# Performance work log

Measured on AMD Instinct MI355X. Metric: run time of the kernel, lower is better.

The kernel has to match this reference:

```python
import jax, jax.numpy as jnp
import numpy as np

DIM = 1024
DFF = 4096
LN_EPS = 1e-5


def _layernorm(x, g, b):
    mu = jnp.mean(x, axis=-1, keepdims=True)
    var = jnp.mean((x - mu) ** 2, axis=-1, keepdims=True)
    return (x - mu) * jax.lax.rsqrt(var + LN_EPS) * g + b


def setup_inputs() -> dict:
    key = jax.random.key(0)
    ks = jax.random.split(key, 16)
    B, L, D, F = 4, 2048, DIM, DFF
    return {
        "x": jax.random.normal(ks[0], (B, L, D), dtype=jnp.float32),
        "hidden_real": jax.random.normal(ks[1], (B, D), dtype=jnp.float32),
        "hidden_imag": jax.random.normal(ks[2], (B, D), dtype=jnp.float32),
        # SConvLayer params (real/imag pairs, mirroring torch.view_as_real storage)
        "phazor_init": jax.random.normal(ks[3], (D, 2), dtype=jnp.float32),
        "phazor": jax.random.normal(ks[4], (D, 2), dtype=jnp.float32),
        # fc (gate) linear
        "fc_w": jax.random.normal(ks[5], (D, D), dtype=jnp.float32) / np.sqrt(D),
        "fc_b": jax.random.normal(ks[6], (D,), dtype=jnp.float32) * 0.01,
        # FFN
        "w1": jax.random.normal(ks[7], (F, D), dtype=jnp.float32) / np.sqrt(D),
        "b1": jax.random.normal(ks[8], (F,), dtype=jnp.float32) * 0.01,
        "w2": jax.random.normal(ks[9], (D, F), dtype=jnp.float32) / np.sqrt(F),
        "b2": jax.random.normal(ks[10], (D,), dtype=jnp.float32) * 0.01,
        # shared LayerNorm (used twice in the block with the same params)
        "ln_g": jnp.ones((D,), dtype=jnp.float32),
        "ln_b": jnp.zeros((D,), dtype=jnp.float32),
    }


def reference(x, hidden_real, hidden_imag, phazor_init, phazor,
              fc_w, fc_b, w1, b1, w2, b2, ln_g, ln_b):
    B, L, D = x.shape
    hidden = (hidden_real + 1j * hidden_imag).astype(jnp.complex64)

    x_res = x
    xn = _layernorm(x, ln_g, ln_b)

    # --- SConvLayer ---
    pz = (phazor[:, 0] + 1j * phazor[:, 1]).astype(jnp.complex64)  # [D]
    # magnitude exp(-|z|^2), phase = angle(z)
    p = jnp.exp(-(pz.real ** 2 + pz.imag ** 2)) * jnp.exp(1j * jnp.angle(pz))
    t = jnp.arange(L)
    prog = p[None, :] ** t[:, None]                      # [L, D] complex
    init_c = (phazor_init[:, 0] + 1j * phazor_init[:, 1]).astype(jnp.complex64)
    filt = prog * init_c[None, :]                        # [L, D]
    n2 = 2 * L
    filt_fft = jnp.fft.fft(filt, n=n2, axis=0)           # [2L, D]
    x_fft = jnp.fft.fft(xn.astype(jnp.complex64), n=n2, axis=1)  # [B, 2L, D]
    conv = jnp.fft.ifft(filt_fft[None] * x_fft, axis=1)[:, :L]   # [B, L, D]
    conv_with_past = conv + hidden[:, None, :] * prog[None] * p[None, None, :]
    sx = conv_with_past.real

    # --- gate ---
    y = jax.nn.silu(jnp.einsum('bld,ed->ble', x_res, fc_w) + fc_b)
    x2 = sx * y + x_res

    # --- FFN (same LayerNorm params) ---
    x3 = _layernorm(x2, ln_g, ln_b)
    h = jax.nn.silu(jnp.einsum('bld,fd->blf', x3, w1) + b1)
    out = jnp.einsum('blf,df->bld', h, w2) + b2 + x2
    return out, conv_with_past
```

## Files before the change

### kernel.cpp

```cpp
#include <hip/hip_runtime.h>
#include <hip/hip_bf16.h>

#define D_MODEL 1024
#define D_FF    4096
#define SEQ_LEN 2048
#define NBATCH  4
#define NROWS   (NBATCH*SEQ_LEN)
#define NCHUNK  32
#define CHUNK_L (SEQ_LEN/NCHUNK)
#define LN_EPS  1e-5f

typedef __hip_bfloat16 bf16;
typedef __attribute__((ext_vector_type(8))) short bf16x8;
typedef __attribute__((ext_vector_type(4))) float f32x4;

__device__ __forceinline__ void gload16(const bf16* g, bf16* l) {
    __builtin_amdgcn_global_load_lds(
        (const __attribute__((address_space(1))) void*)g,
        (__attribute__((address_space(3))) void*)l, 16, 0, 0);
}

__global__ void cast4(const float4* __restrict__ in, ushort4* __restrict__ out, int n4) {
    int i = blockIdx.x * blockDim.x + threadIdx.x;
    if (i < n4) {
        float4 v = in[i];
        union { ushort4 u; bf16 b[4]; } cv;
        cv.b[0] = __float2bfloat16(v.x); cv.b[1] = __float2bfloat16(v.y);
        cv.b[2] = __float2bfloat16(v.z); cv.b[3] = __float2bfloat16(v.w);
        out[i] = cv.u;
    }
}

__global__ void compute_pvec(const float* __restrict__ phz, float* __restrict__ pv) {
    int d = blockIdx.x * blockDim.x + threadIdx.x;
    if (d >= D_MODEL) return;
    float re = phz[2*d], im = phz[2*d+1];
    float r2 = re*re + im*im;
    float mag = expf(-r2);
    float pr, pim;
    if (r2 > 0.f) { float inv = mag / sqrtf(r2); pr = re*inv; pim = im*inv; }
    else          { pr = mag; pim = 0.f; }
    float ar = pr, ai = pim;
    #pragma unroll
    for (int i = 0; i < 6; i++) { float nr = ar*ar - ai*ai; float ni = 2.f*ar*ai; ar = nr; ai = ni; }
    pv[d]            = pr;
    pv[D_MODEL+d]    = pim;
    pv[2*D_MODEL+d]  = ar;
    pv[3*D_MODEL+d]  = ai;
}

__global__ __launch_bounds__(256) void ln_fused(const float* __restrict__ x,
                                                const float* __restrict__ g,
                                                const float* __restrict__ bta,
                                                float* __restrict__ outf,
                                                bf16*  __restrict__ outb,
                                                bf16*  __restrict__ rawb)
{
    int row = blockIdx.x;
    int tid = threadIdx.x;
    const float4* xr = (const float4*)(x + (size_t)row * D_MODEL);
    float4 v = xr[tid];
    if (rawb) {
        union { ushort4 u; bf16 b[4]; } cv;
        cv.b[0]=__float2bfloat16(v.x); cv.b[1]=__float2bfloat16(v.y);
        cv.b[2]=__float2bfloat16(v.z); cv.b[3]=__float2bfloat16(v.w);
        ((ushort4*)(rawb + (size_t)row * D_MODEL))[tid] = cv.u;
    }
    float s  = v.x + v.y + v.z + v.w;
    float s2 = v.x*v.x + v.y*v.y + v.z*v.z + v.w*v.w;
    for (int off = 32; off; off >>= 1) { s += __shfl_down(s, off); s2 += __shfl_down(s2, off); }
    __shared__ float red[8];
    int wid = tid >> 6, lane = tid & 63;
    if (lane == 0) { red[wid] = s; red[4+wid] = s2; }
    __syncthreads();
    if (tid == 0) {
        red[0] = red[0]+red[1]+red[2]+red[3];
        red[4] = red[4]+red[5]+red[6]+red[7];
    }
    __syncthreads();
    float mu  = red[0] * (1.f/D_MODEL);
    float var = red[4] * (1.f/D_MODEL) - mu*mu;
    float rstd = rsqrtf(var + LN_EPS);
    float4 gv = ((const float4*)g)[tid];
    float4 bv = ((const float4*)bta)[tid];
    float4 o;
    o.x = (v.x-mu)*rstd*gv.x + bv.x;
    o.y = (v.y-mu)*rstd*gv.y + bv.y;
    o.z = (v.z-mu)*rstd*gv.z + bv.z;
    o.w = (v.w-mu)*rstd*gv.w + bv.w;
    if (outf) ((float4*)(outf + (size_t)row * D_MODEL))[tid] = o;
    if (outb) {
        union { ushort4 u; bf16 b[4]; } cv;
        cv.b[0]=__float2bfloat16(o.x); cv.b[1]=__float2bfloat16(o.y);
        cv.b[2]=__float2bfloat16(o.z); cv.b[3]=__float2bfloat16(o.w);
        ((ushort4*)(outb + (size_t)row * D_MODEL))[tid] = cv.u;
    }
}

__global__ __launch_bounds__(256) void scan_pass1(const float* __restrict__ xn,
                                                  const float* __restrict__ pv,
                                                  const float* __restrict__ pini,
                                                  float* __restrict__ Sc)
{
    int d = blockIdx.x * 256 + threadIdx.x;
    int c = blockIdx.y, b = blockIdx.z;
    float pr = pv[d], pim = pv[D_MODEL+d];
    float icr = pini[2*d], ici = pini[2*d+1];
    float Sr = 0.f, Si = 0.f;
    const float* xp = xn + ((size_t)b*SEQ_LEN + c*CHUNK_L) * D_MODEL + d;
    #pragma unroll 8
    for (int i = 0; i < CHUNK_L; i++) {
        float xv = xp[(size_t)i * D_MODEL];
        float nr = pr*Sr - pim*Si + icr*xv;
        float ni = pr*Si + pim*Sr + ici*xv;
        Sr = nr; Si = ni;
    }
    size_t o = ((size_t)b*NCHUNK + c) * D_MODEL + d;
    Sc[2*o] = Sr; Sc[2*o+1] = Si;
}

__global__ __launch_bounds__(256) void scan_prefix(const float* __restrict__ Sc,
                                                   const float* __restrict__ pv,
                                                   const float* __restrict__ hr,
                                                   const float* __restrict__ hi,
                                                   float* __restrict__ pref)
{
    int d = blockIdx.x * 256 + threadIdx.x;
    int b = blockIdx.y;
    float qr = pv[2*D_MODEL+d], qi = pv[3*D_MODEL+d];
    float Ur = hr[b*D_MODEL+d], Ui = hi[b*D_MODEL+d];
    for (int c = 0; c < NCHUNK; c++) {
        size_t o = ((size_t)b*NCHUNK + c) * D_MODEL + d;
        pref[2*o] = Ur; pref[2*o+1] = Ui;
        float sr = Sc[2*o], si = Sc[2*o+1];
        float nr = qr*Ur - qi*Ui + sr;
        float ni = qr*Ui + qi*Ur + si;
        Ur = nr; Ui = ni;
    }
}

__global__ __launch_bounds__(256) void scan_pass2(const float* __restrict__ xn,
                                                  const float* __restrict__ pv,
                                                  const float* __restrict__ pini,
                                                  const float* __restrict__ pref,
                                                  float* __restrict__ cwp,
                                                  int interleaved)
{
    int d = blockIdx.x * 256 + threadIdx.x;
    int c = blockIdx.y, b = blockIdx.z;
    float pr = pv[d], pim = pv[D_MODEL+d];
    float icr = pini[2*d], ici = pini[2*d+1];
    size_t po = ((size_t)b*NCHUNK + c) * D_MODEL + d;
    float Ur = pref[2*po], Ui = pref[2*po+1];
    size_t base = ((size_t)b*SEQ_LEN + c*CHUNK_L) * D_MODEL + d;
    const float* xp = xn + base;
    if (interleaved) {
        float2* cp = (float2*)cwp + base;
        #pragma unroll 8
        for (int i = 0; i < CHUNK_L; i++) {
            float xv = xp[(size_t)i * D_MODEL];
            float nr = pr*Ur - pim*Ui + icr*xv;
            float ni = pr*Ui + pim*Ur + ici*xv;
            Ur = nr; Ui = ni;
            cp[(size_t)i * D_MODEL] = make_float2(Ur, Ui);
        }
    } else {
        float* cp = cwp + base;
        #pragma unroll 8
        for (int i = 0; i < CHUNK_L; i++) {
            float xv = xp[(size_t)i * D_MODEL];
            float nr = pr*Ur - pim*Ui + icr*xv;
            float ni = pr*Ui + pim*Ur + ici*xv;
            Ur = nr; Ui = ni;
            cp[(size_t)i * D_MODEL] = Ur;
        }
    }
}

#define BM 128
#define BN 128
#define BK 32

template<int EPI>
__global__ __launch_bounds__(256) void gemm_bt(const bf16* __restrict__ A,
                                               const bf16* __restrict__ Bt,
                                               const float* __restrict__ bias,
                                               const float* __restrict__ e0, int e0_stride,
                                               const float* __restrict__ e1,
                                               float* __restrict__ outf,
                                               bf16*  __restrict__ outb,
                                               int M, int N, int K)
{
    __shared__ __align__(16) bf16 As[3][BM*BK];
    __shared__ __align__(16) bf16 Bs[3][BM*BK];
    int tid = threadIdx.x;
    int m0 = blockIdx.x * BM;
    int n0 = blockIdx.y * BN;

    int wid = tid >> 6, lane = tid & 63;
    int wm = (wid >> 1) * 64, wn = (wid & 1) * 64;
    int lr = lane & 15;
    int lkc = lane >> 4;

    int rl = lane >> 2;
    int cS = (lane & 3) ^ ((rl >> 1) & 3);
    const bf16* gA0 = A  + (size_t)(m0 +      wid*16 + rl) * K + cS*8;
    const bf16* gA1 = A  + (size_t)(m0 + 64 + wid*16 + rl) * K + cS*8;
    const bf16* gB0 = Bt + (size_t)(n0 +      wid*16 + rl) * K + cS*8;
    const bf16* gB1 = Bt + (size_t)(n0 + 64 + wid*16 + rl) * K + cS*8;
    int lo0 = (     wid*16) * BK;
    int lo1 = (64 + wid*16) * BK;

    int keyr = (lr >> 1) & 3;
    int cR = (lkc ^ keyr) * 8;
    int offA[4], offB[4];
    #pragma unroll
    for (int i = 0; i < 4; i++) {
        offA[i] = (wm + i*16 + lr) * BK + cR;
        offB[i] = (wn + i*16 + lr) * BK + cR;
    }

    int nt = K / BK;
    auto stage = [&](int slot, int tile) {
        int k0 = tile * BK;
        gload16(gA0 + k0, &As[slot][lo0]);
        gload16(gA1 + k0, &As[slot][lo1]);
        gload16(gB0 + k0, &Bs[slot][lo0]);
        gload16(gB1 + k0, &Bs[slot][lo1]);
    };
    f32x4 acc[4][4] = {};
    auto compute = [&](int slot) {
        bf16x8 af[4], bfv[4];
        #pragma unroll
        for (int i = 0; i < 4; i++) {
            af[i]  = *(const bf16x8*)&As[slot][offA[i]];
            bfv[i] = *(const bf16x8*)&Bs[slot][offB[i]];
        }
        #pragma unroll
        for (int i = 0; i < 4; i++)
            #pragma unroll
            for (int j = 0; j < 4; j++)
                acc[i][j] = __builtin_amdgcn_mfma_f32_16x16x32_bf16(af[i], bfv[j], acc[i][j], 0, 0, 0);
    };

    stage(0, 0); stage(1, 1); stage(2, 2);

    int s = 0;
    for (int t = 0; t < nt - 3; ++t) {
        asm volatile("s_waitcnt vmcnt(8)" ::: "memory");
        __builtin_amdgcn_s_barrier();
        __builtin_amdgcn_sched_barrier(0);
        compute(s);
        asm volatile("" ::: "memory");
        __builtin_amdgcn_s_barrier();
        stage(s, t + 3);
        s = (s == 2) ? 0 : s + 1;
    }
    asm volatile("s_waitcnt vmcnt(8)" ::: "memory");
    __builtin_amdgcn_s_barrier();
    __builtin_amdgcn_sched_barrier(0);
    compute(s);
    s = (s == 2) ? 0 : s + 1;
    asm volatile("s_waitcnt vmcnt(4)" ::: "memory");
    __builtin_amdgcn_s_barrier();
    __builtin_amdgcn_sched_barrier(0);
    compute(s);
    s = (s == 2) ? 0 : s + 1;
    asm volatile("s_waitcnt vmcnt(0)" ::: "memory");
    __builtin_amdgcn_s_barrier();
    __builtin_amdgcn_sched_barrier(0);
    compute(s);

    int mrow = 4 * (lane >> 4);
    #pragma unroll
    for (int i = 0; i < 4; i++) {
        #pragma unroll
        for (int j = 0; j < 4; j++) {
            int nb = n0 + wn + j*16 + lr;
            float bb = bias[nb];
            #pragma unroll
            for (int r = 0; r < 4; r++) {
                int m = m0 + wm + i*16 + mrow + r;
                size_t idx = (size_t)m * N + nb;
                float v = acc[i][j][r] + bb;
                if (EPI == 0) {
                    float yv = v / (1.f + __expf(-v));
                    float sxv = e0[idx * (size_t)e0_stride];
                    outf[idx] = sxv * yv + e1[idx];
                } else if (EPI == 1) {
                    float yv = v / (1.f + __expf(-v));
                    outb[idx] = __float2bfloat16(yv);
                } else {
                    outf[idx] = v + e0[idx];
                }
            }
        }
    }
}

extern "C" void kernel_launch(void* const* d_in, const int* in_sizes, int n_in,
                              void* d_out, int out_size, void* d_ws, size_t ws_size,
                              hipStream_t stream)
{
    const float* x    = (const float*)d_in[0];
    const float* hr   = (const float*)d_in[1];
    const float* hi   = (const float*)d_in[2];
    const float* pini = (const float*)d_in[3];
    const float* phz  = (const float*)d_in[4];
    const float* fcw  = (const float*)d_in[5];
    const float* fcb  = (const float*)d_in[6];
    const float* w1   = (const float*)d_in[7];
    const float* b1   = (const float*)d_in[8];
    const float* w2   = (const float*)d_in[9];
    const float* b2   = (const float*)d_in[10];
    const float* lng  = (const float*)d_in[11];
    const float* lnb  = (const float*)d_in[12];

    float* out = (float*)d_out;
    float* cwp = out + (size_t)NROWS * D_MODEL;
    int interleaved = (out_size >= NROWS * D_MODEL * 3) ? 1 : 0;

    char* ws = (char*)d_ws;
    size_t off = 0;
    bf16*  wfcb = (bf16*)(ws + off);  off += (size_t)D_MODEL*D_MODEL*2;
    bf16*  w1b  = (bf16*)(ws + off);  off += (size_t)D_FF*D_MODEL*2;
    bf16*  w2b  = (bf16*)(ws + off);  off += (size_t)D_MODEL*D_FF*2;
    float* pv   = (float*)(ws + off); off += (size_t)4*D_MODEL*4;
    float* xn   = (float*)(ws + off); off += (size_t)NROWS*D_MODEL*4;
    bf16*  xbf  = (bf16*)(ws + off);  off += (size_t)NROWS*D_MODEL*2;
    float* Sc   = (float*)(ws + off); off += (size_t)NBATCH*NCHUNK*D_MODEL*2*4;
    float* pref = (float*)(ws + off); off += (size_t)NBATCH*NCHUNK*D_MODEL*2*4;
    float* x2   = (float*)(ws + off); off += (size_t)NROWS*D_MODEL*4;
    bf16*  x3b  = (bf16*)(ws + off);  off += (size_t)NROWS*D_MODEL*2;
    bf16*  hbuf = (bf16*)(ws + off);  off += (size_t)NROWS*D_FF*2;

    cast4<<<1024, 256, 0, stream>>>((const float4*)fcw, (ushort4*)wfcb, D_MODEL*D_MODEL/4);
    cast4<<<4096, 256, 0, stream>>>((const float4*)w1,  (ushort4*)w1b,  D_FF*D_MODEL/4);
    cast4<<<4096, 256, 0, stream>>>((const float4*)w2,  (ushort4*)w2b,  D_MODEL*D_FF/4);

    compute_pvec<<<4, 256, 0, stream>>>(phz, pv);

    ln_fused<<<NROWS, 256, 0, stream>>>(x, lng, lnb, xn, nullptr, xbf);

    scan_pass1<<<dim3(4, NCHUNK, NBATCH), 256, 0, stream>>>(xn, pv, pini, Sc);
    scan_prefix<<<dim3(4, NBATCH), 256, 0, stream>>>(Sc, pv, hr, hi, pref);
    scan_pass2<<<dim3(4, NCHUNK, NBATCH), 256, 0, stream>>>(xn, pv, pini, pref, cwp, interleaved);

    gemm_bt<0><<<dim3(NROWS/BM, D_MODEL/BN), 256, 0, stream>>>(
        xbf, wfcb, fcb, cwp, interleaved ? 2 : 1, x, x2, nullptr, NROWS, D_MODEL, D_MODEL);

    ln_fused<<<NROWS, 256, 0, stream>>>(x2, lng, lnb, nullptr, x3b, nullptr);

    gemm_bt<1><<<dim3(NROWS/BM, D_FF/BN), 256, 0, stream>>>(
        x3b, w1b, b1, nullptr, 1, nullptr, nullptr, hbuf, NROWS, D_FF, D_MODEL);

    gemm_bt<2><<<dim3(NROWS/BM, D_MODEL/BN), 256, 0, stream>>>(
        hbuf, w2b, b2, x2, 1, nullptr, out, nullptr, NROWS, D_MODEL, D_FF);
}
```

Measured before the change: 274.7 us.

## Use 256x256 tiled GEMM with 8 waves for the FFN up-projection

```diff
diff --git a/kernel.cpp b/kernel.cpp
--- a/kernel.cpp
+++ b/kernel.cpp
@@ -177,6 +177,23 @@
     }
 }
 
+template<int EPI>
+__device__ __forceinline__ void epi_store(float v, size_t idx,
+                                          const float* e0, int e0_stride, const float* e1,
+                                          float* outf, bf16* outb)
+{
+    if (EPI == 0) {
+        float yv = v / (1.f + __expf(-v));
+        float sxv = e0[idx * (size_t)e0_stride];
+        outf[idx] = sxv * yv + e1[idx];
+    } else if (EPI == 1) {
+        float yv = v / (1.f + __expf(-v));
+        outb[idx] = __float2bfloat16(yv);
+    } else {
+        outf[idx] = v + e0[idx];
+    }
+}
+
 #define BM 128
 #define BN 128
 #define BK 32
@@ -282,17 +299,116 @@
             for (int r = 0; r < 4; r++) {
                 int m = m0 + wm + i*16 + mrow + r;
                 size_t idx = (size_t)m * N + nb;
-                float v = acc[i][j][r] + bb;
-                if (EPI == 0) {
-                    float yv = v / (1.f + __expf(-v));
-                    float sxv = e0[idx * (size_t)e0_stride];
-                    outf[idx] = sxv * yv + e1[idx];
-                } else if (EPI == 1) {
-                    float yv = v / (1.f + __expf(-v));
-                    outb[idx] = __float2bfloat16(yv);
-                } else {
-                    outf[idx] = v + e0[idx];
-                }
+                epi_store<EPI>(acc[i][j][r] + bb, idx, e0, e0_stride, e1, outf, outb);
+            }
+        }
+    }
+}
+
+#define TM 256
+#define TN 256
+
+template<int EPI>
+__global__ __launch_bounds__(512, 2) void gemm256(const bf16* __restrict__ A,
+                                                  const bf16* __restrict__ Bt,
+                                                  const float* __restrict__ bias,
+                                                  const float* __restrict__ e0, int e0_stride,
+                                                  const float* __restrict__ e1,
+                                                  float* __restrict__ outf,
+                                                  bf16*  __restrict__ outb,
+                                                  int M, int N, int K)
+{
+    __shared__ __align__(16) bf16 As[3][TM*BK];
+    __shared__ __align__(16) bf16 Bs[3][TN*BK];
+    int tid = threadIdx.x;
+    int m0 = blockIdx.x * TM;
+    int n0 = blockIdx.y * TN;
+
+    int wid = tid >> 6, lane = tid & 63;
+    int wr = wid >> 2, wc = wid & 3;
+    int wm = wr * 128, wn = wc * 64;
+    int lr = lane & 15;
+    int lkc = lane >> 4;
+
+    int rl = tid >> 2;
+    int cS = (tid & 3) ^ ((rl >> 1) & 3);
+    const bf16* gA0 = A  + (size_t)(m0 +       rl) * K + cS*8;
+    const bf16* gA1 = A  + (size_t)(m0 + 128 + rl) * K + cS*8;
+    const bf16* gB0 = Bt + (size_t)(n0 +       rl) * K + cS*8;
+    const bf16* gB1 = Bt + (size_t)(n0 + 128 + rl) * K + cS*8;
+    int lo0 = (      wid*16) * BK;
+    int lo1 = (128 + wid*16) * BK;
+
+    int keyr = (lr >> 1) & 3;
+    int cR = (lkc ^ keyr) * 8;
+    int offA[8], offB[4];
+    #pragma unroll
+    for (int i = 0; i < 8; i++) offA[i] = (wm + i*16 + lr) * BK + cR;
+    #pragma unroll
+    for (int j = 0; j < 4; j++) offB[j] = (wn + j*16 + lr) * BK + cR;
+
+    int nt = K / BK;
+    auto stage = [&](int slot, int tile) {
+        int k0 = tile * BK;
+        gload16(gA0 + k0, &As[slot][lo0]);
+        gload16(gA1 + k0, &As[slot][lo1]);
+        gload16(gB0 + k0, &Bs[slot][lo0]);
+        gload16(gB1 + k0, &Bs[slot][lo1]);
+    };
+    f32x4 acc[8][4] = {};
+    auto compute = [&](int slot) {
+        bf16x8 af[8], bfv[4];
+        #pragma unroll
+        for (int i = 0; i < 8; i++) af[i]  = *(const bf16x8*)&As[slot][offA[i]];
+        #pragma unroll
+        for (int j = 0; j < 4; j++) bfv[j] = *(const bf16x8*)&Bs[slot][offB[j]];
+        #pragma unroll
+        for (int i = 0; i < 8; i++)
+            #pragma unroll
+            for (int j = 0; j < 4; j++)
+                acc[i][j] = __builtin_amdgcn_mfma_f32_16x16x32_bf16(af[i], bfv[j], acc[i][j], 0, 0, 0);
+    };
+
+    stage(0, 0); stage(1, 1); stage(2, 2);
+
+    int s = 0;
+    for (int t = 0; t < nt - 3; ++t) {
+        asm volatile("s_waitcnt vmcnt(8)" ::: "memory");
+        __builtin_amdgcn_s_barrier();
+        __builtin_amdgcn_sched_barrier(0);
+        compute(s);
+        asm volatile("" ::: "memory");
+        __builtin_amdgcn_s_barrier();
+        stage(s, t + 3);
+        s = (s == 2) ? 0 : s + 1;
+    }
+    asm volatile("s_waitcnt vmcnt(8)" ::: "memory");
+    __builtin_amdgcn_s_barrier();
+    __builtin_amdgcn_sched_barrier(0);
+    compute(s);
+    s = (s == 2) ? 0 : s + 1;
+    asm volatile("s_waitcnt vmcnt(4)" ::: "memory");
+    __builtin_amdgcn_s_barrier();
+    __builtin_amdgcn_sched_barrier(0);
+    compute(s);
+    s = (s == 2) ? 0 : s + 1;
+    asm volatile("s_waitcnt vmcnt(0)" ::: "memory");
+    __builtin_amdgcn_s_barrier();
+    __builtin_amdgcn_sched_barrier(0);
+    compute(s);
+
+    int mrow = 4 * (lane >> 4);
+    #pragma unroll
+    for (int i = 0; i < 8; i++) {
+        #pragma unroll
+        for (int j = 0; j < 4; j++) {
+            int nb = n0 + wn + j*16 + lr;
+            float bb = bias[nb];
+            #pragma unroll
+            for (int r = 0; r < 4; r++) {
+                int m = m0 + wm + i*16 + mrow + r;
+                size_t idx = (size_t)m * N + nb;
+                epi_store<EPI>(acc[i][j][r] + bb, idx, e0, e0_stride, e1, outf, outb);
             }
         }
     }
@@ -351,7 +467,7 @@
 
     ln_fused<<<NROWS, 256, 0, stream>>>(x2, lng, lnb, nullptr, x3b, nullptr);
 
-    gemm_bt<1><<<dim3(NROWS/BM, D_FF/BN), 256, 0, stream>>>(
+    gemm256<1><<<dim3(NROWS/TM, D_FF/TN), 512, 0, stream>>>(
         x3b, w1b, b1, nullptr, 1, nullptr, nullptr, hbuf, NROWS, D_FF, D_MODEL);
 
     gemm_bt<2><<<dim3(NROWS/BM, D_MODEL/BN), 256, 0, stream>>>(
```

Measured after the change: 271.8 us. Within noise of the previous version (-1.1%).
